# Kernel optimization log

Measured on AMD Instinct MI355X. Metric: run time of the kernel, lower is better.

The kernel has to match this reference:

```python
import jax, jax.numpy as jnp
import numpy as np

B, S, D, H = 1024, 64, 1024, 32
HD = D // H  # 32


def make_rpe_map():
    # one-hot map from 225 relative offsets (15x15) to 64x64 (q,k) board pairs
    out = np.zeros((225, 64 * 64), dtype=np.float32)
    for i in range(8):
        for j in range(8):
            for k in range(8):
                for m in range(8):
                    out[15 * (i - k + 7) + (j - m + 7), 64 * (i * 8 + j) + k * 8 + m] = 1
    return out


RPE_MAP = jnp.asarray(make_rpe_map())  # [225, 4096]


def setup_inputs() -> dict:
    key = jax.random.key(0)
    ks = jax.random.split(key, 11)
    s = 0.02
    return {
        "x": jax.random.normal(ks[0], (B, S, D), jnp.float32),
        "q_w": jax.random.normal(ks[1], (D, D), jnp.float32) * s,
        "q_b": jax.random.normal(ks[2], (D,), jnp.float32) * s,
        "k_w": jax.random.normal(ks[3], (D, D), jnp.float32) * s,
        "k_b": jax.random.normal(ks[4], (D,), jnp.float32) * s,
        "v_w": jax.random.normal(ks[5], (D, D), jnp.float32) * s,
        "v_b": jax.random.normal(ks[6], (D,), jnp.float32) * s,
        "out_w": jax.random.normal(ks[7], (D, D), jnp.float32) * s,
        "out_b": jax.random.normal(ks[8], (D,), jnp.float32) * s,
        "rpe_q_w": jax.random.normal(ks[9], (HD * H, 225), jnp.float32) * s,
        "rpe_k_w": jax.random.normal(ks[10], (HD * H, 225), jnp.float32) * s,
    }


def reference(x, q_w, q_b, k_w, k_b, v_w, v_b, out_w, out_b, rpe_q_w, rpe_k_w):
    b, s, _ = x.shape

    def proj(w, bias):
        # torch Linear: y = x @ w.T + b ; then [B,S,H,HD] -> [B,H,S,HD]
        return (x @ w.T + bias).reshape(b, s, H, HD).transpose(0, 2, 1, 3)

    q = proj(q_w, q_b)
    k = proj(k_w, k_b)
    v = proj(v_w, v_b)

    scores = jnp.einsum('bhqd,bhkd->bhqk', q, k)
    bias_q = (rpe_q_w @ RPE_MAP).reshape(HD, H, 64, 64)  # [d,h,q,k]
    scores = scores + jnp.einsum('bhqd,dhqk->bhqk', q, bias_q)
    bias_k = (rpe_k_w @ RPE_MAP).reshape(HD, H, 64, 64)
    scores = scores + jnp.einsum('bhkd,dhqk->bhqk', k, bias_k)
    scores = scores / jnp.sqrt(jnp.asarray(HD, scores.dtype))

    attn = jax.nn.softmax(scores, axis=-1)
    out = jnp.einsum('bhqk,bhkd->bhqd', attn, v)
    out = out.transpose(0, 2, 1, 3).reshape(b, s, D)
    return out @ out_w.T + out_b
```

## Files before the change

kernel.cpp:

```cpp
#include <hip/hip_runtime.h>
#include <hip/hip_bf16.h>

#define AS1 __attribute__((address_space(1)))
#define AS3 __attribute__((address_space(3)))

typedef __attribute__((ext_vector_type(4))) float f32x4;
typedef __attribute__((ext_vector_type(8))) short b16x8;
typedef __attribute__((ext_vector_type(8))) unsigned short u16x8;
typedef unsigned short u16;

static __device__ __forceinline__ u16 f2b(float f) {
  return __builtin_bit_cast(u16, __float2bfloat16(f));
}
static __device__ __forceinline__ float b2f(u16 u) {
  unsigned v = ((unsigned)u) << 16;
  return __builtin_bit_cast(float, v);
}
static __device__ __forceinline__ void gl2lds16(const u16* g, u16* l) {
  __builtin_amdgcn_global_load_lds((const AS1 void*)g, (AS3 void*)l, 16, 0, 0);
}

__global__ void k_cvt(const float* __restrict__ s, u16* __restrict__ d, long n) {
  long i = ((long)blockIdx.x * 256 + threadIdx.x) * 8;
  if (i >= n) return;
  float4 a = *(const float4*)(s + i);
  float4 b = *(const float4*)(s + i + 4);
  u16x8 o;
  o[0] = f2b(a.x); o[1] = f2b(a.y); o[2] = f2b(a.z); o[3] = f2b(a.w);
  o[4] = f2b(b.x); o[5] = f2b(b.y); o[6] = f2b(b.z); o[7] = f2b(b.w);
  *(u16x8*)(d + i) = o;
}

__global__ void k_rpe(const float* __restrict__ rq, const float* __restrict__ rk,
                      u16* __restrict__ oq, u16* __restrict__ ok) {
  int h = blockIdx.y;
  int r = blockIdx.x * 8 + (threadIdx.x >> 5);
  int d = threadIdx.x & 31;
  const float* s = blockIdx.z ? rk : rq;
  u16* o = blockIdx.z ? ok : oq;
  float v = (r < 225) ? s[(d * 32 + h) * 225 + r] : 0.f;
  o[(h * 240 + r) * 32 + d] = f2b(v);
}

template <int MODE>
__global__ __launch_bounds__(512) void k_gemm(
    const u16* __restrict__ A, const u16* __restrict__ Bw,
    const float* __restrict__ b0, const float* __restrict__ b1, const float* __restrict__ b2,
    u16* __restrict__ oq, float* __restrict__ of) {
  __shared__ alignas(16) u16 lds[4][16384];
  const int tid = threadIdx.x;
  const int l = tid & 63, w = tid >> 6;
  const int lo = l & 15, hi = l >> 4;
  const int wr = w >> 2, wc = w & 3;

  const int nbx = gridDim.x;
  const int nb = nbx * gridDim.y;
  const int bid = blockIdx.y * nbx + blockIdx.x;
  const int ord = (bid & 7) * (nb >> 3) + (bid >> 3);
  const int tn = (ord % nbx) * 256, tm = (ord / nbx) * 256;

  const int sl = (tid & 7) ^ ((tid >> 3) & 7);
  const int srow = 2 * (tid >> 3) + (sl >> 2);
  const int scol = (sl & 3) * 8;
  const u16* gA = A + (size_t)(tm + srow) * 1024 + scol;
  const u16* gB = Bw + (size_t)(tn + srow) * 1024 + scol;
  u16* dst = &lds[0][0] + tid * 8;

  const int p7 = (lo >> 1) & 7;
  const int slr = ((lo & 1) * 4 + hi) ^ p7;
  const int aoff = wr * 4096 + (lo >> 1) * 64 + slr * 8;
  const int boff = 8192 + wc * 2048 + (lo >> 1) * 64 + slr * 8;

  f32x4 acc[8][4];
#pragma unroll
  for (int i = 0; i < 8; ++i)
#pragma unroll
    for (int j = 0; j < 4; ++j) acc[i][j] = (f32x4){0.f, 0.f, 0.f, 0.f};

#define STG(t) { const int kc = (t) * 32; u16* d = dst + ((t) & 3) * 16384; \
    gl2lds16(gA + kc, d);           gl2lds16(gA + 131072 + kc, d + 4096); \
    gl2lds16(gB + kc, d + 8192);    gl2lds16(gB + 131072 + kc, d + 12288); }
#define RDF(fa, fb, bi) { const u16* _b = &lds[0][0] + (bi) * 16384; \
    _Pragma("unroll") for (int _i = 0; _i < 8; ++_i) fa[_i] = *(const b16x8*)(_b + aoff + _i * 512); \
    _Pragma("unroll") for (int _j = 0; _j < 4; ++_j) fb[_j] = *(const b16x8*)(_b + boff + _j * 512); }
#define MMS(fa, fb) { __builtin_amdgcn_s_setprio(1); \
    _Pragma("unroll") for (int _i = 0; _i < 8; ++_i) \
    _Pragma("unroll") for (int _j = 0; _j < 4; ++_j) \
      acc[_i][_j] = __builtin_amdgcn_mfma_f32_16x16x32_bf16(fa[_i], fb[_j], acc[_i][_j], 0, 0, 0); \
    __builtin_amdgcn_s_setprio(0); }
#define WB(n) { asm volatile("s_waitcnt vmcnt(" #n ")" ::: "memory"); \
    __builtin_amdgcn_s_barrier(); asm volatile("" ::: "memory"); }

  b16x8 fa0[8], fb0[4], fa1[8], fb1[4];

  STG(0) STG(1) STG(2)
  WB(4)
  RDF(fa0, fb0, 0)

  for (int kt = 0; kt < 28; kt += 2) {
    STG(kt + 3)
    RDF(fa1, fb1, (kt + 1) & 3)
    MMS(fa0, fb0)
    WB(4)
    STG(kt + 4)
    RDF(fa0, fb0, (kt + 2) & 3)
    MMS(fa1, fb1)
    WB(4)
  }
  STG(31)
  RDF(fa1, fb1, 1)
  MMS(fa0, fb0)
  WB(4)
  RDF(fa0, fb0, 2)
  MMS(fa1, fb1)
  WB(0)
  RDF(fa1, fb1, 3)
  MMS(fa0, fb0)
  MMS(fa1, fb1)
#undef STG
#undef RDF
#undef MMS
#undef WB

  if (MODE == 0) {
    const size_t G = 67108864;
    const int g = tn >> 10;
    const float* bias = (g == 0) ? b0 : (g == 1) ? b1 : b2;
    const int nn0 = (tn & 1023) + wc * 64;
#pragma unroll
    for (int j = 0; j < 4; ++j) {
      const int nn = nn0 + j * 16 + lo;
      const float bv = bias[nn];
      const int h = nn >> 5, hd = nn & 31;
      if (g < 2) {
#pragma unroll
        for (int i = 0; i < 8; ++i) {
          const int m0 = tm + wr * 128 + i * 16 + hi * 4;
          const int b = m0 >> 6, s0 = m0 & 63;
          const size_t base = (size_t)g * G + ((size_t)(b * 32 + h) * 64 + s0) * 32 + hd;
#pragma unroll
          for (int r = 0; r < 4; ++r) oq[base + (size_t)r * 32] = f2b(acc[i][j][r] + bv);
        }
      } else {
#pragma unroll
        for (int i = 0; i < 8; ++i) {
          const int m0 = tm + wr * 128 + i * 16 + hi * 4;
          const int b = m0 >> 6, s0 = m0 & 63;
          ushort4 pk;
          pk.x = f2b(acc[i][j][0] + bv);
          pk.y = f2b(acc[i][j][1] + bv);
          pk.z = f2b(acc[i][j][2] + bv);
          pk.w = f2b(acc[i][j][3] + bv);
          *(ushort4*)(oq + 2 * G + ((size_t)(b * 32 + h) * 32 + hd) * 64 + s0) = pk;
        }
      }
    }
  } else {
#pragma unroll
    for (int j = 0; j < 4; ++j) {
      const int n = tn + wc * 64 + j * 16 + lo;
      const float bv = b0[n];
#pragma unroll
      for (int i = 0; i < 8; ++i) {
        const int m0 = tm + wr * 128 + i * 16 + hi * 4;
#pragma unroll
        for (int r = 0; r < 4; ++r) of[(size_t)(m0 + r) * 1024 + n] = acc[i][j][r] + bv;
      }
    }
  }
}

__global__ __launch_bounds__(256) void k_attn(
    const u16* __restrict__ qkv, const u16* __restrict__ rq,
    const u16* __restrict__ rk, u16* __restrict__ att) {
  __shared__ alignas(16) u16 board[16 * 240 * 4];
  u16* pl = board;
  const int l = threadIdx.x & 63, w = threadIdx.x >> 6;
  const int lo = l & 15, hi = l >> 4;
  const int b = blockIdx.x, h = blockIdx.y;
  const size_t G = 67108864;
  const u16* qp = qkv + (size_t)(b * 32 + h) * 2048;
  const u16* kp = qkv + G + (size_t)(b * 32 + h) * 2048;
  const u16* vp = qkv + 2 * G + (size_t)(b * 32 + h) * 2048;

  b16x8 qf = *(const b16x8*)(qp + (w * 16 + lo) * 32 + hi * 8);
  b16x8 v00 = *(const b16x8*)(vp + lo * 64 + hi * 8);
  b16x8 v01 = *(const b16x8*)(vp + lo * 64 + 32 + hi * 8);
  b16x8 v10 = *(const b16x8*)(vp + (16 + lo) * 64 + hi * 8);
  b16x8 v11 = *(const b16x8*)(vp + (16 + lo) * 64 + 32 + hi * 8);

  f32x4 s0[4];
#pragma unroll
  for (int kt = 0; kt < 4; ++kt) {
    b16x8 kf = *(const b16x8*)(kp + (kt * 16 + lo) * 32 + hi * 8);
    f32x4 z = (f32x4){0.f, 0.f, 0.f, 0.f};
    s0[kt] = __builtin_amdgcn_mfma_f32_16x16x32_bf16(qf, kf, z, 0, 0, 0);
  }

  const u16* rqh = rq + (size_t)h * 7680;
#pragma unroll
  for (int nt = 0; nt < 15; ++nt) {
    b16x8 rf = *(const b16x8*)(rqh + (nt * 16 + lo) * 32 + hi * 8);
    f32x4 z = (f32x4){0.f, 0.f, 0.f, 0.f};
    f32x4 c = __builtin_amdgcn_mfma_f32_16x16x32_bf16(qf, rf, z, 0, 0, 0);
    ushort4 pk;
    pk.x = f2b(c[0]); pk.y = f2b(c[1]); pk.z = f2b(c[2]); pk.w = f2b(c[3]);
    *(ushort4*)(board + (((w * 4 + hi) * 240 + nt * 16 + lo) << 2)) = pk;
  }
#pragma unroll
  for (int kt = 0; kt < 4; ++kt)
#pragma unroll
    for (int r = 0; r < 4; ++r) {
      int q = w * 16 + hi * 4 + r, k = kt * 16 + lo;
      int rel = 15 * ((q >> 3) - (k >> 3) + 7) + (q & 7) - (k & 7) + 7;
      s0[kt][r] += b2f(board[((w * 4 + hi) * 240 + rel) * 4 + r]);
    }

  b16x8 kfa = *(const b16x8*)(kp + (w * 16 + lo) * 32 + hi * 8);
  const u16* rkh = rk + (size_t)h * 7680;
#pragma unroll
  for (int nt = 0; nt < 15; ++nt) {
    b16x8 rf = *(const b16x8*)(rkh + (nt * 16 + lo) * 32 + hi * 8);
    f32x4 z = (f32x4){0.f, 0.f, 0.f, 0.f};
    f32x4 c = __builtin_amdgcn_mfma_f32_16x16x32_bf16(kfa, rf, z, 0, 0, 0);
    ushort4 pk;
    pk.x = f2b(c[0]); pk.y = f2b(c[1]); pk.z = f2b(c[2]); pk.w = f2b(c[3]);
    *(ushort4*)(board + (((w * 4 + hi) * 240 + nt * 16 + lo) << 2)) = pk;
  }
  __syncthreads();
#pragma unroll
  for (int kt = 0; kt < 4; ++kt)
#pragma unroll
    for (int r = 0; r < 4; ++r) {
      int q = w * 16 + hi * 4 + r, k = kt * 16 + lo;
      int rel = 15 * ((q >> 3) - (k >> 3) + 7) + (q & 7) - (k & 7) + 7;
      s0[kt][r] += b2f(board[((k >> 2) * 240 + rel) * 4 + (k & 3)]);
    }

  const float sc = 0.17677669529663689f;
#pragma unroll
  for (int kt = 0; kt < 4; ++kt) s0[kt] *= sc;
  float p[4][4], rsum[4];
#pragma unroll
  for (int r = 0; r < 4; ++r) {
    float m = s0[0][r];
    m = fmaxf(m, s0[1][r]); m = fmaxf(m, s0[2][r]); m = fmaxf(m, s0[3][r]);
    m = fmaxf(m, __shfl_xor(m, 1));
    m = fmaxf(m, __shfl_xor(m, 2));
    m = fmaxf(m, __shfl_xor(m, 4));
    m = fmaxf(m, __shfl_xor(m, 8));
    float sum = 0.f;
#pragma unroll
    for (int kt = 0; kt < 4; ++kt) {
      float e = __expf(s0[kt][r] - m);
      p[kt][r] = e;
      sum += e;
    }
    sum += __shfl_xor(sum, 1);
    sum += __shfl_xor(sum, 2);
    sum += __shfl_xor(sum, 4);
    sum += __shfl_xor(sum, 8);
    rsum[r] = 1.f / sum;
  }

  __syncthreads();

#pragma unroll
  for (int kt = 0; kt < 4; ++kt)
#pragma unroll
    for (int r = 0; r < 4; ++r) pl[(w * 16 + hi * 4 + r) * 72 + kt * 16 + lo] = f2b(p[kt][r]);

  f32x4 o0 = (f32x4){0.f, 0.f, 0.f, 0.f}, o1 = (f32x4){0.f, 0.f, 0.f, 0.f};
  {
    b16x8 pa0 = *(const b16x8*)(pl + (w * 16 + lo) * 72 + hi * 8);
    b16x8 pa1 = *(const b16x8*)(pl + (w * 16 + lo) * 72 + 32 + hi * 8);
    o0 = __builtin_amdgcn_mfma_f32_16x16x32_bf16(pa0, v00, o0, 0, 0, 0);
    o1 = __builtin_amdgcn_mfma_f32_16x16x32_bf16(pa0, v10, o1, 0, 0, 0);
    o0 = __builtin_amdgcn_mfma_f32_16x16x32_bf16(pa1, v01, o0, 0, 0, 0);
    o1 = __builtin_amdgcn_mfma_f32_16x16x32_bf16(pa1, v11, o1, 0, 0, 0);
  }

#pragma unroll
  for (int r = 0; r < 4; ++r) {
    int q = w * 16 + hi * 4 + r;
    size_t base = (size_t)(b * 64 + q) * 1024 + h * 32;
    att[base + lo] = f2b(o0[r] * rsum[r]);
    att[base + 16 + lo] = f2b(o1[r] * rsum[r]);
  }
}

extern "C" void kernel_launch(void* const* d_in, const int* in_sizes, int n_in,
                              void* d_out, int out_size, void* d_ws, size_t ws_size,
                              hipStream_t stream) {
  const float* x   = (const float*)d_in[0];
  const float* qw  = (const float*)d_in[1];
  const float* qb  = (const float*)d_in[2];
  const float* kw  = (const float*)d_in[3];
  const float* kb  = (const float*)d_in[4];
  const float* vw  = (const float*)d_in[5];
  const float* vb  = (const float*)d_in[6];
  const float* ow  = (const float*)d_in[7];
  const float* ob  = (const float*)d_in[8];
  const float* rqw = (const float*)d_in[9];
  const float* rkw = (const float*)d_in[10];

  if (ws_size < 680460288ULL) return;
  char* p = (char*)d_ws;
  u16* ws_x   = (u16*)p; p += (size_t)65536 * 1024 * 2;
  u16* ws_w   = (u16*)p; p += (size_t)3 * 1024 * 1024 * 2;
  u16* ws_wo  = (u16*)p; p += (size_t)1024 * 1024 * 2;
  u16* ws_rq  = (u16*)p; p += (size_t)32 * 240 * 32 * 2;
  u16* ws_rk  = (u16*)p; p += (size_t)32 * 240 * 32 * 2;
  u16* ws_qkv = (u16*)p; p += (size_t)3 * 67108864 * 2;
  u16* ws_att = (u16*)p; p += (size_t)65536 * 1024 * 2;

  k_cvt<<<32768, 256, 0, stream>>>(x, ws_x, 67108864L);
  k_cvt<<<512, 256, 0, stream>>>(qw, ws_w, 1048576L);
  k_cvt<<<512, 256, 0, stream>>>(kw, ws_w + 1048576, 1048576L);
  k_cvt<<<512, 256, 0, stream>>>(vw, ws_w + 2097152, 1048576L);
  k_cvt<<<512, 256, 0, stream>>>(ow, ws_wo, 1048576L);
  k_rpe<<<dim3(30, 32, 2), 256, 0, stream>>>(rqw, rkw, ws_rq, ws_rk);

  k_gemm<0><<<dim3(12, 256), 512, 0, stream>>>(ws_x, ws_w, qb, kb, vb, ws_qkv, nullptr);
  k_attn<<<dim3(1024, 32), 256, 0, stream>>>(ws_qkv, ws_rq, ws_rk, ws_att);
  k_gemm<1><<<dim3(4, 256), 512, 0, stream>>>(ws_att, ws_wo, ob, nullptr, nullptr, nullptr,
                                              (float*)d_out);
}
```

Before: 1.020 ms.

## Restructure GEMM main loop into two-phase ping-pong with split A/B staging

Replaces the double-buffered register fragment scheme (two sets of A/B fragments with read-ahead) with a single fragment set processed in two half-phases per k-tile. Each phase loads part of the fragments, synchronises the block with barriers, waits on LDS, then issues its MFMAs at raised priority. Global-to-LDS staging is split into separate A and B issues placed between the phases. The aim is to interleave memory and matrix work across waves and cut register pressure. The cost is extra barriers per k-tile and a different vmcnt accounting that must match the new issue order.

```diff
diff --git a/kernel.cpp b/kernel.cpp
--- a/kernel.cpp
+++ b/kernel.cpp
@@ -77,50 +77,59 @@
 #pragma unroll
     for (int j = 0; j < 4; ++j) acc[i][j] = (f32x4){0.f, 0.f, 0.f, 0.f};
 
-#define STG(t) { const int kc = (t) * 32; u16* d = dst + ((t) & 3) * 16384; \
-    gl2lds16(gA + kc, d);           gl2lds16(gA + 131072 + kc, d + 4096); \
-    gl2lds16(gB + kc, d + 8192);    gl2lds16(gB + 131072 + kc, d + 12288); }
-#define RDF(fa, fb, bi) { const u16* _b = &lds[0][0] + (bi) * 16384; \
-    _Pragma("unroll") for (int _i = 0; _i < 8; ++_i) fa[_i] = *(const b16x8*)(_b + aoff + _i * 512); \
-    _Pragma("unroll") for (int _j = 0; _j < 4; ++_j) fb[_j] = *(const b16x8*)(_b + boff + _j * 512); }
-#define MMS(fa, fb) { __builtin_amdgcn_s_setprio(1); \
-    _Pragma("unroll") for (int _i = 0; _i < 8; ++_i) \
+  b16x8 af[8], bf[4];
+
+#define STG_A(t) { const int kc = (t) * 32; u16* d = dst + ((t) & 3) * 16384; \
+    gl2lds16(gA + kc, d);  gl2lds16(gA + 131072 + kc, d + 4096); }
+#define STG_B(t) { const int kc = (t) * 32; u16* d = dst + ((t) & 3) * 16384; \
+    gl2lds16(gB + kc, d + 8192);  gl2lds16(gB + 131072 + kc, d + 12288); }
+#define PHA(bi) { const u16* _b = &lds[0][0] + (bi) * 16384; \
+    _Pragma("unroll") for (int _i = 0; _i < 4; ++_i) af[_i] = *(const b16x8*)(_b + aoff + _i * 512); \
+    _Pragma("unroll") for (int _j = 0; _j < 4; ++_j) bf[_j] = *(const b16x8*)(_b + boff + _j * 512); \
+    __builtin_amdgcn_s_barrier(); \
+    asm volatile("s_waitcnt lgkmcnt(0)" ::: "memory"); \
+    __builtin_amdgcn_sched_barrier(0); \
+    __builtin_amdgcn_s_setprio(1); \
+    _Pragma("unroll") for (int _i = 0; _i < 4; ++_i) \
     _Pragma("unroll") for (int _j = 0; _j < 4; ++_j) \
-      acc[_i][_j] = __builtin_amdgcn_mfma_f32_16x16x32_bf16(fa[_i], fb[_j], acc[_i][_j], 0, 0, 0); \
+      acc[_i][_j] = __builtin_amdgcn_mfma_f32_16x16x32_bf16(af[_i], bf[_j], acc[_i][_j], 0, 0, 0); \
+    __builtin_amdgcn_s_setprio(0); \
+    __builtin_amdgcn_s_barrier(); }
+#define PHB(bi) { const u16* _b = &lds[0][0] + (bi) * 16384; \
+    _Pragma("unroll") for (int _i = 4; _i < 8; ++_i) af[_i] = *(const b16x8*)(_b + aoff + _i * 512); \
+    __builtin_amdgcn_s_barrier(); \
+    asm volatile("s_waitcnt lgkmcnt(0)" ::: "memory"); \
+    __builtin_amdgcn_sched_barrier(0); \
+    __builtin_amdgcn_s_setprio(1); \
+    _Pragma("unroll") for (int _i = 4; _i < 8; ++_i) \
+    _Pragma("unroll") for (int _j = 0; _j < 4; ++_j) \
+      acc[_i][_j] = __builtin_amdgcn_mfma_f32_16x16x32_bf16(af[_i], bf[_j], acc[_i][_j], 0, 0, 0); \
     __builtin_amdgcn_s_setprio(0); }
-#define WB(n) { asm volatile("s_waitcnt vmcnt(" #n ")" ::: "memory"); \
+#define WV(n) { asm volatile("s_waitcnt vmcnt(" #n ")" ::: "memory"); \
     __builtin_amdgcn_s_barrier(); asm volatile("" ::: "memory"); }
 
-  b16x8 fa0[8], fb0[4], fa1[8], fb1[4];
-
-  STG(0) STG(1) STG(2)
-  WB(4)
-  RDF(fa0, fb0, 0)
-
-  for (int kt = 0; kt < 28; kt += 2) {
-    STG(kt + 3)
-    RDF(fa1, fb1, (kt + 1) & 3)
-    MMS(fa0, fb0)
-    WB(4)
-    STG(kt + 4)
-    RDF(fa0, fb0, (kt + 2) & 3)
-    MMS(fa1, fb1)
-    WB(4)
-  }
-  STG(31)
-  RDF(fa1, fb1, 1)
-  MMS(fa0, fb0)
-  WB(4)
-  RDF(fa0, fb0, 2)
-  MMS(fa1, fb1)
-  WB(0)
-  RDF(fa1, fb1, 3)
-  MMS(fa0, fb0)
-  MMS(fa1, fb1)
-#undef STG
-#undef RDF
-#undef MMS
-#undef WB
+  STG_A(0) STG_B(0) STG_A(1) STG_B(1) STG_A(2) STG_B(2)
+  asm volatile("s_waitcnt vmcnt(8)" ::: "memory");
+  __builtin_amdgcn_s_barrier();
+  asm volatile("" ::: "memory");
+
+#pragma unroll 4
+  for (int kt = 0; kt < 28; ++kt) {
+    STG_A(kt + 3)
+    PHA(kt & 3)
+    STG_B(kt + 3)
+    PHB(kt & 3)
+    WV(8)
+  }
+  STG_A(31) PHA(0) STG_B(31) PHB(0) WV(8)
+  PHA(1) PHB(1) WV(4)
+  PHA(2) PHB(2) WV(0)
+  PHA(3) PHB(3)
+#undef STG_A
+#undef STG_B
+#undef PHA
+#undef PHB
+#undef WV
 
   if (MODE == 0) {
     const size_t G = 67108864;
```

After: 1.009 ms. No clear change (-1.1%).
